# Performance work log

Measured on AMD Instinct MI355X. Metric: run time of the kernel, lower is better.

The kernel has to match this reference:

```python
import jax, jax.numpy as jnp
import numpy as np

D_MODEL = 1024
N_HEADS = 16
HEAD_DIM = D_MODEL // N_HEADS
ROPE_BASE = 10000.0


def rotate_half(x):
    x1, x2 = x[..., : x.shape[-1] // 2], x[..., x.shape[-1] // 2 :]
    return jnp.concatenate((-x2, x1), axis=-1)


def rope_cos_sin(L, dim, dtype):
    inv_freq = 1.0 / (ROPE_BASE ** (jnp.arange(0, dim, 2, dtype=jnp.float32) / dim))
    freqs = jnp.arange(L, dtype=jnp.float32)[:, None] * inv_freq[None, :]  # [L, dim/2]
    emb = jnp.concatenate((freqs, freqs), axis=-1)  # [L, dim]
    # broadcast over batch and heads: [1, L, 1, dim]
    return jnp.cos(emb)[None, :, None, :].astype(dtype), jnp.sin(emb)[None, :, None, :].astype(dtype)


def setup_inputs() -> dict:
    key = jax.random.key(0)
    ks = jax.random.split(key, 11)
    N, L, S = 2, 2048, 2048
    s = 1.0 / np.sqrt(D_MODEL)
    return {
        "queries": jax.random.normal(ks[0], (N, L, D_MODEL), jnp.float32),
        "keys": jax.random.normal(ks[1], (N, S, D_MODEL), jnp.float32),
        "values": jax.random.normal(ks[2], (N, S, D_MODEL), jnp.float32),
        "Wq": jax.random.normal(ks[3], (D_MODEL, D_MODEL), jnp.float32) * s,
        "bq": jnp.zeros((D_MODEL,), jnp.float32),
        "Wk": jax.random.normal(ks[4], (D_MODEL, D_MODEL), jnp.float32) * s,
        "bk": jnp.zeros((D_MODEL,), jnp.float32),
        "Wv": jax.random.normal(ks[5], (D_MODEL, D_MODEL), jnp.float32) * s,
        "bv": jnp.zeros((D_MODEL,), jnp.float32),
        "Wo": jax.random.normal(ks[6], (D_MODEL, D_MODEL), jnp.float32) * s,
        "bo": jnp.zeros((D_MODEL,), jnp.float32),
    }


def reference(queries, keys, values, Wq, bq, Wk, bk, Wv, bv, Wo, bo):
    N, L, _ = queries.shape
    S = keys.shape[1]
    H, hd = N_HEADS, HEAD_DIM

    # QKV projections (nn.Linear: x @ W.T + b), reshape to [N, T, H, hd]
    q = (jnp.einsum("nld,ed->nle", queries, Wq) + bq).reshape(N, L, H, hd)
    k = (jnp.einsum("nsd,ed->nse", keys, Wk) + bk).reshape(N, S, H, hd)
    v = (jnp.einsum("nsd,ed->nse", values, Wv) + bv).reshape(N, S, H, hd)

    # Rotary embedding: q*cos + rotate_half(q)*sin  (same for k)
    cos, sin = rope_cos_sin(L, hd, q.dtype)
    q = q * cos + rotate_half(q) * sin
    k = k * cos + rotate_half(k) * sin

    # Inner attention: scaled dot-product with causal mask
    scores = jnp.einsum("nlhd,nshd->nhls", q, k) / jnp.sqrt(jnp.asarray(hd, q.dtype))
    causal = jnp.tril(jnp.ones((L, S), bool))
    scores = jnp.where(causal[None, None], scores, jnp.asarray(-1e9, scores.dtype))
    attn = jax.nn.softmax(scores, axis=-1)
    out = jnp.einsum("nhls,nshd->nlhd", attn, v).reshape(N, L, H * hd)

    # Output projection
    return jnp.einsum("nle,de->nld", out, Wo) + bo
```

## Files before the change

kernel.cpp:

```cpp
#include <hip/hip_runtime.h>
#include <math.h>

#define DM 1024
#define NH 16
#define HD 64
#define SEQ 2048
#define NB2 2
#define MROWS 4096

typedef unsigned short u16;
typedef __attribute__((ext_vector_type(8))) short short8;
typedef __attribute__((ext_vector_type(4))) float f32x4;
typedef __attribute__((ext_vector_type(2))) unsigned int u32x2;

#define GLOAD16(g, l) __builtin_amdgcn_global_load_lds( \
    (const __attribute__((address_space(1))) void*)(g),  \
    (__attribute__((address_space(3))) void*)(l), 16, 0, 0)

static __device__ __forceinline__ u16 f2bf(float f) {
  union { float f; unsigned u; } v; v.f = f;
  unsigned r = v.u + 0x7fffu + ((v.u >> 16) & 1u);
  return (u16)(r >> 16);
}

static __device__ __forceinline__ short8 cvt8(float4 a, float4 b) {
  short8 s;
  s[0] = (short)f2bf(a.x); s[1] = (short)f2bf(a.y);
  s[2] = (short)f2bf(a.z); s[3] = (short)f2bf(a.w);
  s[4] = (short)f2bf(b.x); s[5] = (short)f2bf(b.y);
  s[6] = (short)f2bf(b.z); s[7] = (short)f2bf(b.w);
  return s;
}

__global__ void conv_all(
    const float* __restrict__ q, const float* __restrict__ k, const float* __restrict__ v,
    const float* __restrict__ wq, const float* __restrict__ wk,
    const float* __restrict__ wv, const float* __restrict__ wo,
    u16* __restrict__ xq, u16* __restrict__ xk, u16* __restrict__ xv,
    u16* __restrict__ wqb, u16* __restrict__ wkb, u16* __restrict__ wvb, u16* __restrict__ wob,
    float* __restrict__ cosT, float* __restrict__ sinT)
{
  const int z = blockIdx.z;
  const int idx = blockIdx.x * blockDim.x + threadIdx.x;
  if (z == 7) {
    if (idx >= SEQ * 32) return;
    int l = idx >> 5, i = idx & 31;
    float invf = expf(-(float)i * (9.210340371976184f / 32.0f));
    float ang = (float)l * invf;
    float s, c;
    sincosf(ang, &s, &c);
    cosT[idx] = c; sinT[idx] = s;
    return;
  }
  const float* src; u16* dst; int n;
  switch (z) {
    case 0: src = q;  dst = xq;  n = MROWS * DM; break;
    case 1: src = k;  dst = xk;  n = MROWS * DM; break;
    case 2: src = v;  dst = xv;  n = MROWS * DM; break;
    case 3: src = wq; dst = wqb; n = DM * DM; break;
    case 4: src = wk; dst = wkb; n = DM * DM; break;
    case 5: src = wv; dst = wvb; n = DM * DM; break;
    default: src = wo; dst = wob; n = DM * DM; break;
  }
  const int base = idx * 8;
  if (base >= n) return;
  float4 a = *(const float4*)(src + base);
  float4 b = *(const float4*)(src + base + 4);
  *(short8*)(dst + base) = cvt8(a, b);
}

#define VSTR 136
template<int EPI>
__device__ __forceinline__ void gemm_body(
    u16* SH,
    const u16* __restrict__ A, const u16* __restrict__ W,
    const float* __restrict__ bias,
    u16* __restrict__ Cb, float* __restrict__ Cf, u16* __restrict__ VT,
    const float* __restrict__ cosT, const float* __restrict__ sinT,
    float qscale, int row0, int col0)
{
  u16* As = SH;
  u16* Bs = SH + 4096;
  const int tid = threadIdx.x;
  const int lane = tid & 63;
  const int w = tid >> 6;
  const int wr = w >> 1, wc = w & 1;
  const int fr = lane & 15, kg = lane >> 4;

  const int c0 = w * 128 + lane;
  const int c1 = c0 + 64;
  const u16* ga0 = A + (size_t)(row0 + (c0 & 127)) * DM + ((c0 >> 7) << 3);
  const u16* ga1 = A + (size_t)(row0 + (c1 & 127)) * DM + ((c1 >> 7) << 3);
  const u16* gb0 = W + (size_t)(col0 + (c0 & 127)) * DM + ((c0 >> 7) << 3);
  const u16* gb1 = W + (size_t)(col0 + (c1 & 127)) * DM + ((c1 >> 7) << 3);
  u16* la0 = As + (w * 128) * 8;
  u16* la1 = As + (w * 128 + 64) * 8;
  u16* lb0 = Bs + (w * 128) * 8;
  u16* lb1 = Bs + (w * 128 + 64) * 8;

  f32x4 acc[4][4];
#pragma unroll
  for (int m = 0; m < 4; ++m)
#pragma unroll
    for (int n = 0; n < 4; ++n) acc[m][n] = (f32x4){0.f, 0.f, 0.f, 0.f};

  const int KT = DM / 32;
  for (int kt = 0; kt < KT; ++kt) {
    const int ko = kt * 32;
    GLOAD16(ga0 + ko, la0);
    GLOAD16(ga1 + ko, la1);
    GLOAD16(gb0 + ko, lb0);
    GLOAD16(gb1 + ko, lb1);
    __syncthreads();
    short8 afr[4], bfr[4];
#pragma unroll
    for (int m = 0; m < 4; ++m)
      afr[m] = *(const short8*)(&As[kg * 1024 + (wr * 64 + m * 16 + fr) * 8]);
#pragma unroll
    for (int n = 0; n < 4; ++n)
      bfr[n] = *(const short8*)(&Bs[kg * 1024 + (wc * 64 + n * 16 + fr) * 8]);
#pragma unroll
    for (int m = 0; m < 4; ++m)
#pragma unroll
      for (int n = 0; n < 4; ++n)
        acc[m][n] = __builtin_amdgcn_mfma_f32_16x16x32_bf16(afr[m], bfr[n], acc[m][n], 0, 0, 0);
    __syncthreads();
  }

  if (EPI == 2) {
    const int nb = row0 >> 11;
    const int sbase = row0 & (SEQ - 1);
#pragma unroll
    for (int p = 0; p < 2; ++p) {
      if (wc == p) {
#pragma unroll
        for (int n = 0; n < 4; ++n) {
          const int dcol = n * 16 + fr;
          const float bv = bias[col0 + p * 64 + dcol];
#pragma unroll
          for (int m = 0; m < 4; ++m)
#pragma unroll
            for (int r = 0; r < 4; ++r)
              SH[dcol * VSTR + wr * 64 + m * 16 + kg * 4 + r] = f2bf(acc[m][n][r] + bv);
        }
      }
      __syncthreads();
      {
        const int dcol = tid >> 2, sq = tid & 3;
        const int e = col0 + p * 64 + dcol;
        u16* dst = VT + ((size_t)(nb * NH + (e >> 6)) * HD + (e & 63)) * SEQ + sbase + sq * 32;
#pragma unroll
        for (int i = 0; i < 4; ++i)
          *(short8*)(dst + i * 8) = *(const short8*)(&SH[dcol * VSTR + sq * 32 + i * 8]);
      }
      __syncthreads();
    }
    return;
  }

#pragma unroll
  for (int m = 0; m < 4; ++m) {
#pragma unroll
    for (int r = 0; r < 4; ++r) {
      const int rowg = row0 + wr * 64 + m * 16 + kg * 4 + r;
      if (EPI == 1) {
#pragma unroll
        for (int n = 0; n < 4; ++n) {
          const int colg = col0 + wc * 64 + n * 16 + fr;
          Cf[(size_t)rowg * DM + colg] = acc[m][n][r] + bias[colg];
        }
      } else {
        const int l = rowg & (SEQ - 1);
#pragma unroll
        for (int n = 0; n < 4; ++n) {
          const int colg = col0 + wc * 64 + n * 16 + fr;
          const int i = n * 16 + fr;
          const int fi = i & 31;
          const float c = cosT[l * 32 + fi];
          const float s = sinT[l * 32 + fi];
          const float v = acc[m][n][r] + bias[colg];
          const float pv = acc[m][n ^ 2][r] + bias[col0 + wc * 64 + ((n ^ 2) * 16 + fr)];
          const float o = v * c + ((i < 32) ? -pv : pv) * s;
          Cb[(size_t)rowg * DM + colg] = f2bf(o * qscale);
        }
      }
    }
  }
}

__global__ __launch_bounds__(256) void gemm_qkv(
    const u16* __restrict__ Xq, const u16* __restrict__ Xk, const u16* __restrict__ Xv,
    const u16* __restrict__ Wqb, const u16* __restrict__ Wkb, const u16* __restrict__ Wvb,
    const float* __restrict__ bq, const float* __restrict__ bk, const float* __restrict__ bv,
    u16* __restrict__ Qb, u16* __restrict__ Kb, u16* __restrict__ VT,
    const float* __restrict__ cosT, const float* __restrict__ sinT)
{
  __shared__ __align__(16) u16 SH[64 * VSTR];
  const int z = blockIdx.z;
  const int row0 = blockIdx.x * 128, col0 = blockIdx.y * 128;
  if (z == 2) {
    gemm_body<2>(SH, Xv, Wvb, bv, nullptr, nullptr, VT, nullptr, nullptr, 1.0f, row0, col0);
  } else if (z == 0) {
    gemm_body<0>(SH, Xq, Wqb, bq, Qb, nullptr, nullptr, cosT, sinT, 0.125f, row0, col0);
  } else {
    gemm_body<0>(SH, Xk, Wkb, bk, Kb, nullptr, nullptr, cosT, sinT, 1.0f, row0, col0);
  }
}

__global__ __launch_bounds__(256) void gemm_o(
    const u16* __restrict__ Ob, const u16* __restrict__ Wob,
    const float* __restrict__ bo, float* __restrict__ out)
{
  __shared__ __align__(16) u16 SH[64 * VSTR];
  gemm_body<1>(SH, Ob, Wob, bo, nullptr, out, nullptr, nullptr, nullptr, 1.0f,
               blockIdx.x * 128, blockIdx.y * 128);
}

__global__ __launch_bounds__(512) void flash_attn(
    const u16* __restrict__ Qp, const u16* __restrict__ Kp,
    const u16* __restrict__ VT, u16* __restrict__ Op)
{
  __shared__ __align__(16) u16 Ks[4096];
  __shared__ __align__(16) u16 Vt[4096];
  __shared__ __align__(16) u16 Pl[9216];

  const int tid = threadIdx.x;
  const int lane = tid & 63;
  const int w = tid >> 6;
  const int fr = lane & 15, rg = lane >> 4;
  const int qbp = blockIdx.x;
  const int h = blockIdx.y, nb = blockIdx.z;

  const size_t headoff = (size_t)nb * SEQ * DM + (size_t)h * HD;
  const size_t vthead = (size_t)(nb * NH + h) * HD * SEQ;
  const int srow = tid >> 3;
  const int sch  = tid & 7;
  u16* Pw = &Pl[w * 1152];

  for (int pass = 0; pass < 2; ++pass) {
    const int qe = pass ? (15 - qbp) : qbp;
    const int KBend = 2 * qe + 2;
    const int qrow0 = qe * 128 + w * 16;
    const int qg = qrow0 + fr;

    short8 qf[2];
#pragma unroll
    for (int ck = 0; ck < 2; ++ck)
      qf[ck] = *(const short8*)(Qp + headoff + (size_t)(qrow0 + fr) * DM + ck * 32 + rg * 8);

    f32x4 accO[4];
#pragma unroll
    for (int df = 0; df < 4; ++df) accO[df] = (f32x4){0.f, 0.f, 0.f, 0.f};
    float m_run = -3e38f, l_run = 0.f;

    short8 kpf = *(const short8*)(Kp + headoff + (size_t)srow * DM + sch * 8);
    short8 vpf = *(const short8*)(VT + vthead + (size_t)srow * SEQ + sch * 8);

    for (int kb = 0; kb < KBend; ++kb) {
      *(short8*)(&Ks[(sch * 64 + (srow ^ sch)) * 8]) = kpf;
      *(short8*)(&Vt[(sch * 64 + (srow ^ sch)) * 8]) = vpf;
      __syncthreads();
      if (kb + 1 < KBend) {
        kpf = *(const short8*)(Kp + headoff + (size_t)((kb + 1) * 64 + srow) * DM + sch * 8);
        vpf = *(const short8*)(VT + vthead + (size_t)srow * SEQ + (kb + 1) * 64 + sch * 8);
      }

      const bool active = (kb * 64) <= (qrow0 + 15);
      if (active) {
        short8 kf[4][2];
#pragma unroll
        for (int sf = 0; sf < 4; ++sf)
#pragma unroll
          for (int ck = 0; ck < 2; ++ck) {
            const int dc = ck * 4 + rg;
            kf[sf][ck] = *(const short8*)(&Ks[(dc * 64 + ((sf * 16 + fr) ^ dc)) * 8]);
          }
        f32x4 sc_[4];
#pragma unroll
        for (int sf = 0; sf < 4; ++sf) {
          f32x4 z = (f32x4){0.f, 0.f, 0.f, 0.f};
#pragma unroll
          for (int ck = 0; ck < 2; ++ck)
            z = __builtin_amdgcn_mfma_f32_16x16x32_bf16(kf[sf][ck], qf[ck], z, 0, 0, 0);
          sc_[sf] = z;
        }
        float rowmax = -3e38f;
#pragma unroll
        for (int sf = 0; sf < 4; ++sf)
#pragma unroll
          for (int r = 0; r < 4; ++r) {
            const int sg = kb * 64 + sf * 16 + rg * 4 + r;
            float v = sc_[sf][r];
            v = (sg <= qg) ? v : -3e38f;
            sc_[sf][r] = v;
            rowmax = fmaxf(rowmax, v);
          }
        rowmax = fmaxf(rowmax, __shfl_xor(rowmax, 16, 64));
        rowmax = fmaxf(rowmax, __shfl_xor(rowmax, 32, 64));
        const float mnew = fmaxf(m_run, rowmax);
        const float scl = __expf(m_run - mnew);
        m_run = mnew;
        float psum = 0.f;
#pragma unroll
        for (int sf = 0; sf < 4; ++sf)
#pragma unroll
          for (int r = 0; r < 4; ++r) {
            const float p = __expf(sc_[sf][r] - mnew);
            sc_[sf][r] = p;
            psum += p;
          }
        psum += __shfl_xor(psum, 16, 64);
        psum += __shfl_xor(psum, 32, 64);
        l_run = l_run * scl + psum;
        const float s0 = __shfl(scl, rg * 4 + 0, 64);
        const float s1 = __shfl(scl, rg * 4 + 1, 64);
        const float s2 = __shfl(scl, rg * 4 + 2, 64);
        const float s3 = __shfl(scl, rg * 4 + 3, 64);
#pragma unroll
        for (int df = 0; df < 4; ++df) {
          accO[df][0] *= s0; accO[df][1] *= s1;
          accO[df][2] *= s2; accO[df][3] *= s3;
        }
#pragma unroll
        for (int sf = 0; sf < 4; ++sf) {
          u32x2 pv;
          pv[0] = (unsigned)f2bf(sc_[sf][0]) | ((unsigned)f2bf(sc_[sf][1]) << 16);
          pv[1] = (unsigned)f2bf(sc_[sf][2]) | ((unsigned)f2bf(sc_[sf][3]) << 16);
          *(u32x2*)(&Pw[fr * 72 + (sf * 8 + rg * 2) * 2]) = pv;
        }
        short8 pa[2];
#pragma unroll
        for (int ck = 0; ck < 2; ++ck)
          pa[ck] = *(const short8*)(&Pw[fr * 72 + (ck * 16 + rg * 4) * 2]);
#pragma unroll
        for (int df = 0; df < 4; ++df)
#pragma unroll
          for (int ck = 0; ck < 2; ++ck) {
            const int sc = ck * 4 + rg;
            const short8 vf = *(const short8*)(&Vt[(sc * 64 + ((df * 16 + fr) ^ sc)) * 8]);
            accO[df] = __builtin_amdgcn_mfma_f32_16x16x32_bf16(pa[ck], vf, accO[df], 0, 0, 0);
          }
      }
      __syncthreads();
    }

    const float l0 = __shfl(l_run, rg * 4 + 0, 64);
    const float l1 = __shfl(l_run, rg * 4 + 1, 64);
    const float l2 = __shfl(l_run, rg * 4 + 2, 64);
    const float l3 = __shfl(l_run, rg * 4 + 3, 64);
#pragma unroll
    for (int df = 0; df < 4; ++df) {
      const int d = df * 16 + fr;
      Op[headoff + (size_t)(qrow0 + rg * 4 + 0) * DM + d] = f2bf(accO[df][0] / l0);
      Op[headoff + (size_t)(qrow0 + rg * 4 + 1) * DM + d] = f2bf(accO[df][1] / l1);
      Op[headoff + (size_t)(qrow0 + rg * 4 + 2) * DM + d] = f2bf(accO[df][2] / l2);
      Op[headoff + (size_t)(qrow0 + rg * 4 + 3) * DM + d] = f2bf(accO[df][3] / l3);
    }
  }
}

extern "C" void kernel_launch(void* const* d_in, const int* in_sizes, int n_in,
                              void* d_out, int out_size, void* d_ws, size_t ws_size,
                              hipStream_t stream) {
  (void)in_sizes; (void)n_in; (void)out_size; (void)ws_size;
  const float* queries = (const float*)d_in[0];
  const float* keys    = (const float*)d_in[1];
  const float* values  = (const float*)d_in[2];
  const float* Wq = (const float*)d_in[3];
  const float* bq = (const float*)d_in[4];
  const float* Wk = (const float*)d_in[5];
  const float* bk = (const float*)d_in[6];
  const float* Wv = (const float*)d_in[7];
  const float* bv = (const float*)d_in[8];
  const float* Wo = (const float*)d_in[9];
  const float* bo = (const float*)d_in[10];
  float* out = (float*)d_out;

  char* ws = (char*)d_ws;
  const size_t MB = 1u << 20;
  u16* Qb  = (u16*)(ws);
  u16* Kb  = (u16*)(ws + 8 * MB);
  u16* VTg = (u16*)(ws + 16 * MB);
  u16* Xq  = (u16*)(ws + 24 * MB);
  u16* Ob  = Xq;
  u16* Xk  = (u16*)(ws + 32 * MB);
  u16* Xv  = (u16*)(ws + 40 * MB);
  u16* Wqb = (u16*)(ws + 48 * MB);
  u16* Wkb = (u16*)(ws + 50 * MB);
  u16* Wvb = (u16*)(ws + 52 * MB);
  u16* Wob = (u16*)(ws + 54 * MB);
  float* cosT = (float*)(ws + 56 * MB);
  float* sinT = (float*)(ws + 56 * MB + 256 * 1024);

  conv_all<<<dim3(2048, 1, 8), 256, 0, stream>>>(
      queries, keys, values, Wq, Wk, Wv, Wo,
      Xq, Xk, Xv, Wqb, Wkb, Wvb, Wob, cosT, sinT);
  gemm_qkv<<<dim3(MROWS / 128, DM / 128, 3), 256, 0, stream>>>(
      Xq, Xk, Xv, Wqb, Wkb, Wvb, bq, bk, bv, Qb, Kb, VTg, cosT, sinT);
  flash_attn<<<dim3(SEQ / 256, NH, NB2), 512, 0, stream>>>(Qb, Kb, VTg, Ob);
  gemm_o<<<dim3(MROWS / 128, DM / 128), 256, 0, stream>>>(Ob, Wob, bo, out);
}
```

Before: 164.6 us.

## Triple-buffer GEMM K-loop with async LDS loads and single barrier per step

Replaces the single-buffered GEMM main loop, which waits on its loads with two syncthreads per K step, with a three-stage ring of LDS buffers. Global-to-LDS loads are issued two tiles ahead and gated by vmcnt waits, leaving one barrier per step. The aim is to overlap global memory latency with MFMA work in the QKV and output projections. LDS use per block rises to 48KB, which may lower occupancy.

```diff
diff --git a/kernel.cpp b/kernel.cpp
--- a/kernel.cpp
+++ b/kernel.cpp
@@ -79,8 +79,6 @@
     const float* __restrict__ cosT, const float* __restrict__ sinT,
     float qscale, int row0, int col0)
 {
-  u16* As = SH;
-  u16* Bs = SH + 4096;
   const int tid = threadIdx.x;
   const int lane = tid & 63;
   const int w = tid >> 6;
@@ -93,10 +91,14 @@
   const u16* ga1 = A + (size_t)(row0 + (c1 & 127)) * DM + ((c1 >> 7) << 3);
   const u16* gb0 = W + (size_t)(col0 + (c0 & 127)) * DM + ((c0 >> 7) << 3);
   const u16* gb1 = W + (size_t)(col0 + (c1 & 127)) * DM + ((c1 >> 7) << 3);
-  u16* la0 = As + (w * 128) * 8;
-  u16* la1 = As + (w * 128 + 64) * 8;
-  u16* lb0 = Bs + (w * 128) * 8;
-  u16* lb1 = Bs + (w * 128 + 64) * 8;
+  const int lo0 = (w * 128) * 8;
+  const int lo1 = (w * 128 + 64) * 8;
+  const int aoffL = kg * 1024 + (wr * 64 + fr) * 8;
+  const int boffL = 4096 + kg * 1024 + (wc * 64 + fr) * 8;
+
+  u16* B0 = SH;
+  u16* B1 = SH + 8192;
+  u16* B2 = SH + 16384;
 
   f32x4 acc[4][4];
 #pragma unroll
@@ -104,30 +106,59 @@
 #pragma unroll
     for (int n = 0; n < 4; ++n) acc[m][n] = (f32x4){0.f, 0.f, 0.f, 0.f};
 
-  const int KT = DM / 32;
-  for (int kt = 0; kt < KT; ++kt) {
-    const int ko = kt * 32;
-    GLOAD16(ga0 + ko, la0);
-    GLOAD16(ga1 + ko, la1);
-    GLOAD16(gb0 + ko, lb0);
-    GLOAD16(gb1 + ko, lb1);
-    __syncthreads();
+  auto issue = [&](int t, u16* buf) {
+    const int ko = t * 32;
+    GLOAD16(ga0 + ko, buf + lo0);
+    GLOAD16(ga1 + ko, buf + lo1);
+    GLOAD16(gb0 + ko, buf + 4096 + lo0);
+    GLOAD16(gb1 + ko, buf + 4096 + lo1);
+  };
+  auto compute = [&](const u16* buf) {
     short8 afr[4], bfr[4];
 #pragma unroll
     for (int m = 0; m < 4; ++m)
-      afr[m] = *(const short8*)(&As[kg * 1024 + (wr * 64 + m * 16 + fr) * 8]);
+      afr[m] = *(const short8*)(&buf[aoffL + m * 128]);
 #pragma unroll
     for (int n = 0; n < 4; ++n)
-      bfr[n] = *(const short8*)(&Bs[kg * 1024 + (wc * 64 + n * 16 + fr) * 8]);
+      bfr[n] = *(const short8*)(&buf[boffL + n * 128]);
 #pragma unroll
     for (int m = 0; m < 4; ++m)
 #pragma unroll
       for (int n = 0; n < 4; ++n)
         acc[m][n] = __builtin_amdgcn_mfma_f32_16x16x32_bf16(afr[m], bfr[n], acc[m][n], 0, 0, 0);
+  };
+
+  issue(0, B0);
+  issue(1, B1);
+
+#define STEP4(t, bufR, bufW) do {                                   \
+    asm volatile("s_waitcnt vmcnt(4)" ::: "memory");                \
+    __builtin_amdgcn_sched_barrier(0);                              \
+    __builtin_amdgcn_s_barrier();                                   \
+    __builtin_amdgcn_sched_barrier(0);                              \
+    if ((t) + 2 < 32) issue((t) + 2, bufW);                         \
+    compute(bufR);                                                  \
+  } while (0)
+#define STEP0(t, bufR) do {                                         \
+    asm volatile("s_waitcnt vmcnt(0)" ::: "memory");                \
+    __builtin_amdgcn_sched_barrier(0);                              \
+    __builtin_amdgcn_s_barrier();                                   \
+    __builtin_amdgcn_sched_barrier(0);                              \
+    compute(bufR);                                                  \
+  } while (0)
+
+  for (int t = 0; t < 30; t += 3) {
+    STEP4(t,     B0, B2);
+    STEP4(t + 1, B1, B0);
+    STEP4(t + 2, B2, B1);
+  }
+  STEP4(30, B0, B2);
+  STEP0(31, B1);
+#undef STEP4
+#undef STEP0
+
+  if (EPI == 2) {
     __syncthreads();
-  }
-
-  if (EPI == 2) {
     const int nb = row0 >> 11;
     const int sbase = row0 & (SEQ - 1);
 #pragma unroll
@@ -195,7 +226,7 @@
     u16* __restrict__ Qb, u16* __restrict__ Kb, u16* __restrict__ VT,
     const float* __restrict__ cosT, const float* __restrict__ sinT)
 {
-  __shared__ __align__(16) u16 SH[64 * VSTR];
+  __shared__ __align__(16) u16 SH[24576];
   const int z = blockIdx.z;
   const int row0 = blockIdx.x * 128, col0 = blockIdx.y * 128;
   if (z == 2) {
@@ -211,7 +242,7 @@
     const u16* __restrict__ Ob, const u16* __restrict__ Wob,
     const float* __restrict__ bo, float* __restrict__ out)
 {
-  __shared__ __align__(16) u16 SH[64 * VSTR];
+  __shared__ __align__(16) u16 SH[24576];
   gemm_body<1>(SH, Ob, Wob, bo, nullptr, out, nullptr, nullptr, nullptr, 1.0f,
                blockIdx.x * 128, blockIdx.y * 128);
 }
```

Result: faster. 141.3 us (-14.1%).
